# Kernel tuning notes

Measured on AMD Instinct MI355X. Metric: run time of the kernel, lower is better.

The kernel has to match this reference:

```python
import math
import jax, jax.numpy as jnp
import numpy as np

N_TOKENS = 2048
HIDDEN = 2880
HEAD_DIM = 64
N_HEADS = 64
N_KV = 8
Q_MULT = N_HEADS // N_KV  # 8
SLIDING_WINDOW = 128      # layer_idx=0 -> even -> window active
RMS_EPS = 1e-5
SM_SCALE = 1.0 / math.sqrt(HEAD_DIM)
ROPE_THETA = 150000.0
INIT_CTX = 4096
SCALING_FACTOR = 32.0
NTK_ALPHA = 1.0
NTK_BETA = 32.0
QKV_DIM = HEAD_DIM * (N_HEADS + 2 * N_KV)  # 5120


def _rope_cos_sin(n_tokens):
    # YaRN/NTK-scaled inverse frequencies (scaling_factor > 1 branch)
    freq = ROPE_THETA ** (jnp.arange(0, HEAD_DIM, 2, dtype=jnp.float32) / HEAD_DIM)
    concentration = 0.1 * math.log(SCALING_FACTOR) + 1.0
    d_half = HEAD_DIM / 2
    low = d_half * math.log(INIT_CTX / (NTK_BETA * 2 * math.pi)) / math.log(ROPE_THETA)
    high = d_half * math.log(INIT_CTX / (NTK_ALPHA * 2 * math.pi)) / math.log(ROPE_THETA)
    interpolation = 1.0 / (SCALING_FACTOR * freq)
    extrapolation = 1.0 / freq
    ramp = (jnp.arange(d_half, dtype=jnp.float32) - low) / (high - low)
    mask = 1.0 - jnp.clip(ramp, 0.0, 1.0)
    inv_freq = interpolation * (1.0 - mask) + extrapolation * mask
    pos = jnp.arange(n_tokens, dtype=jnp.float32)
    freqs = pos[:, None] * inv_freq[None, :]        # [n, d/2]
    return jnp.cos(freqs) * concentration, jnp.sin(freqs) * concentration


def _apply_rotary(x, cos, sin):
    # x: [n, h, d]; cos/sin: [n, d/2]
    c = cos[:, None, :]
    s = sin[:, None, :]
    x1, x2 = jnp.split(x, 2, axis=-1)
    return jnp.concatenate([x1 * c - x2 * s, x2 * c + x1 * s], axis=-1)


def setup_inputs() -> dict:
    key = jax.random.key(0)
    ks = jax.random.split(key, 4)
    x = jax.random.normal(ks[0], (N_TOKENS, HIDDEN), dtype=jnp.float32)
    norm_scale = jnp.ones((HIDDEN,), dtype=jnp.float32)
    sinks = jax.random.normal(ks[1], (N_HEADS,), dtype=jnp.float32)
    w_qkv = jax.random.normal(ks[2], (QKV_DIM, HIDDEN), dtype=jnp.float32) * 0.02
    b_qkv = jnp.zeros((QKV_DIM,), dtype=jnp.float32)
    w_out = jax.random.normal(ks[3], (HIDDEN, N_HEADS * HEAD_DIM), dtype=jnp.float32) * 0.02
    b_out = jnp.zeros((HIDDEN,), dtype=jnp.float32)
    return {"x": x, "norm_scale": norm_scale, "sinks": sinks,
            "w_qkv": w_qkv, "b_qkv": b_qkv, "w_out": w_out, "b_out": b_out}


def reference(x, norm_scale, sinks, w_qkv, b_qkv, w_out, b_out):
    n = x.shape[0]
    # RMSNorm (fp32 math as in original)
    t = x.astype(jnp.float32)
    t = t * jax.lax.rsqrt(jnp.mean(t * t, axis=-1, keepdims=True) + RMS_EPS)
    t = (t * norm_scale).astype(x.dtype)
    # QKV projection (torch Linear: y = x @ W^T + b)
    qkv = t @ w_qkv.T + b_qkv
    q = qkv[:, : N_HEADS * HEAD_DIM].reshape(n, N_KV, Q_MULT, HEAD_DIM)
    k = qkv[:, N_HEADS * HEAD_DIM:(N_HEADS + N_KV) * HEAD_DIM].reshape(n, N_KV, HEAD_DIM)
    v = qkv[:, (N_HEADS + N_KV) * HEAD_DIM:].reshape(n, N_KV, HEAD_DIM)
    # RoPE
    cos, sin = _rope_cos_sin(n)
    q = _apply_rotary(q.reshape(n, N_HEADS, HEAD_DIM), cos, sin).reshape(n, N_KV, Q_MULT, HEAD_DIM)
    k = _apply_rotary(k, cos, sin)
    # GQA attention scores: [kv_heads, q_mult, q, k]
    qk = jnp.einsum('qhmd,khd->hmqk', q, k) * SM_SCALE
    # causal + sliding-window mask: allow j <= i and j > i - SLIDING_WINDOW
    i = jnp.arange(n)[:, None]
    j = jnp.arange(n)[None, :]
    allowed = (j <= i) & (j > i - SLIDING_WINDOW)
    neg_inf = jnp.asarray(-jnp.inf, dtype=qk.dtype)
    qk = jnp.where(allowed[None, None, :, :], qk, neg_inf)
    # append learned sink logit per head, softmax, then drop sink column
    sink_logits = jnp.broadcast_to(
        sinks.reshape(N_KV, Q_MULT, 1, 1), (N_KV, Q_MULT, n, 1)).astype(qk.dtype)
    logits = jnp.concatenate([qk, sink_logits], axis=-1)
    weights = jax.nn.softmax(logits, axis=-1)[..., :-1]
    attn = jnp.einsum('hmqk,khd->qhmd', weights, v).reshape(n, N_HEADS * HEAD_DIM)
    return x + attn @ w_out.T + b_out
```

## Files before the change

### kernel.cpp

```cpp
#include <hip/hip_runtime.h>
#include <hip/hip_bf16.h>
#include <math.h>

typedef __attribute__((ext_vector_type(8))) short short8;
typedef __attribute__((ext_vector_type(4))) float f32x4;

#define NTOK 2048
#define HID  2880
#define QKVD 5120
#define KOFF 4096
#define VOFF 4608
#define ATTD 4096

__device__ __forceinline__ unsigned short f2bf(float f) {
  union { float f; unsigned int u; } v; v.f = f;
  unsigned int u = v.u;
  unsigned int r = (u + 0x7FFFu + ((u >> 16) & 1u)) >> 16;
  return (unsigned short)r;
}
__device__ __forceinline__ float bf2f(unsigned short h) {
  union { unsigned int u; float f; } v; v.u = ((unsigned int)h) << 16; return v.f;
}
__device__ __forceinline__ void gload_lds16(const unsigned short* g, unsigned short* l) {
  __builtin_amdgcn_global_load_lds(
      (const __attribute__((address_space(1))) unsigned int*)g,
      (__attribute__((address_space(3))) unsigned int*)l, 16, 0, 0);
}
#define MFMA16(a, b, c) __builtin_amdgcn_mfma_f32_16x16x32_bf16((a), (b), (c), 0, 0, 0)

__global__ __launch_bounds__(256) void prep_kernel(
    const float* __restrict__ x, const float* __restrict__ scale,
    unsigned short* __restrict__ t,
    const float* __restrict__ w1, unsigned short* __restrict__ w1bf,
    float* __restrict__ ctab, float* __restrict__ stab) {
  __shared__ float red[4];
  const int bid = blockIdx.x;
  const int tid = threadIdx.x;
  if (bid < 2048) {
    const float4* xr = (const float4*)(x + (size_t)bid * HID);
    const float4* sc = (const float4*)scale;
    float ss = 0.f;
    for (int c = tid; c < HID / 4; c += 256) {
      float4 v = xr[c];
      ss += v.x * v.x + v.y * v.y + v.z * v.z + v.w * v.w;
    }
    #pragma unroll
    for (int m = 1; m < 64; m <<= 1) ss += __shfl_xor(ss, m);
    if ((tid & 63) == 0) red[tid >> 6] = ss;
    __syncthreads();
    float tot = red[0] + red[1] + red[2] + red[3];
    float rs = rsqrtf(tot / (float)HID + 1e-5f);
    for (int c = tid; c < HID / 4; c += 256) {
      float4 v = xr[c];
      float4 s4 = sc[c];
      ushort4 o;
      o.x = f2bf(v.x * rs * s4.x); o.y = f2bf(v.y * rs * s4.y);
      o.z = f2bf(v.z * rs * s4.z); o.w = f2bf(v.w * rs * s4.w);
      *(ushort4*)&t[(size_t)bid * HID + c * 4] = o;
    }
  } else if (bid < 5648) {
    long base0 = (long)(bid - 2048) * 1024;
    #pragma unroll
    for (int k2 = 0; k2 < 4; ++k2) {
      long base = (base0 + k2 * 256 + tid) * 4;
      float4 v = *(const float4*)&w1[base];
      ushort4 o;
      o.x = f2bf(v.x); o.y = f2bf(v.y); o.z = f2bf(v.z); o.w = f2bf(v.w);
      *(ushort4*)&w1bf[base] = o;
    }
  } else {
    int idx = (bid - 5648) * 256 + tid;
    int pos = idx >> 5, i = idx & 31;
    const double theta = 150000.0;
    const double two_pi = 6.283185307179586476925286766559;
    double freq = pow(theta, (double)i / 32.0);
    double interp = 1.0 / (32.0 * freq);
    double extrap = 1.0 / freq;
    double low  = 32.0 * log(4096.0 / (32.0 * two_pi)) / log(theta);
    double high = 32.0 * log(4096.0 / (1.0  * two_pi)) / log(theta);
    double ramp = ((double)i - low) / (high - low);
    ramp = ramp < 0.0 ? 0.0 : (ramp > 1.0 ? 1.0 : ramp);
    double maskv = 1.0 - ramp;
    double inv = interp * (1.0 - maskv) + extrap * maskv;
    double ang = (double)pos * inv;
    double conc = 0.1 * log(32.0) + 1.0;
    ctab[idx] = (float)(cos(ang) * conc);
    stab[idx] = (float)(sin(ang) * conc);
  }
}

template<int BN, bool RESID>
__global__ __launch_bounds__(256, 2) void gemm_kernel(
    const unsigned short* __restrict__ A, const unsigned short* __restrict__ B,
    const float* __restrict__ bias, const float* __restrict__ resid,
    void* __restrict__ Cout, int K, int NC,
    const float* __restrict__ cvt_src, unsigned short* __restrict__ cvt_dst,
    int ngemm) {
  constexpr int NF = BN / 32;
  __shared__ unsigned short sA[2][8192];
  __shared__ unsigned short sB[2][BN * 64];

  const int tid = threadIdx.x;
  if ((int)blockIdx.x >= ngemm) {
    long base0 = (long)((int)blockIdx.x - ngemm) * 1024;
    #pragma unroll
    for (int k2 = 0; k2 < 4; ++k2) {
      long base = (base0 + k2 * 256 + tid) * 4;
      float4 v = *(const float4*)&cvt_src[base];
      ushort4 o;
      o.x = f2bf(v.x); o.y = f2bf(v.y); o.z = f2bf(v.z); o.w = f2bf(v.w);
      *(ushort4*)&cvt_dst[base] = o;
    }
    return;
  }
  const int q8 = ngemm >> 3;
  const int sw = ((int)blockIdx.x & 7) * q8 + ((int)blockIdx.x >> 3);
  const int m0 = (sw & 15) * 128;
  const int n0 = (sw >> 4) * BN;

  const int lane = tid & 63, wid = tid >> 6;
  const int fr = lane & 15, fq = lane >> 4;
  const int wr = wid >> 1, wc = wid & 1;
  const int swz = (fr & 7) << 4;
  const int r_st = tid >> 3;
  const int c8_st = ((tid & 7) ^ ((tid >> 3) & 7)) * 8;
  const int wlds = wid << 9;

  const unsigned short* Ag = A + (size_t)(m0 + r_st) * K + c8_st;
  const unsigned short* Bg = B + (size_t)(n0 + r_st) * K + c8_st;

  f32x4 acc[4][NF] = {};
  const int NT = K >> 6;

  auto LDA_ = [&](int bs, int mf, int ks) -> short8 {
    int row = wr * 64 + mf * 16 + fr;
    int cb = (ks * 64 + fq * 16) ^ swz;
    return *(const short8*)((const char*)&sA[bs][0] + row * 128 + cb);
  };
  auto LDB_ = [&](int bs, int nf, int ks) -> short8 {
    int row = wc * (NF * 16) + nf * 16 + fr;
    int cb = (ks * 64 + fq * 16) ^ swz;
    return *(const short8*)((const char*)&sB[bs][0] + row * 128 + cb);
  };
  auto issue_tile = [&](int tt, int b) {
    const unsigned short* Agt = Ag + (size_t)tt * 64;
    const unsigned short* Bgt = Bg + (size_t)tt * 64;
    #pragma unroll
    for (int s = 0; s < 4; ++s)
      gload_lds16(Agt + (size_t)(s * 32) * K, &sA[b][s * 2048 + wlds]);
    #pragma unroll
    for (int s = 0; s < NF; ++s)
      gload_lds16(Bgt + (size_t)(s * 32) * K, &sB[b][s * 2048 + wlds]);
  };

  issue_tile(0, 0);

  for (int t = 0; t < NT; ++t) {
    const int cu = t & 1;
    asm volatile("s_waitcnt vmcnt(0)" ::: "memory");
    __builtin_amdgcn_s_barrier();
    __builtin_amdgcn_sched_barrier(0);
    if (t + 1 < NT) issue_tile(t + 1, cu ^ 1);
    short8 afr0[4], bfr0[NF], afr1[4], bfr1[NF];
    #pragma unroll
    for (int mf = 0; mf < 4; ++mf) afr0[mf] = LDA_(cu, mf, 0);
    #pragma unroll
    for (int nf = 0; nf < NF; ++nf) bfr0[nf] = LDB_(cu, nf, 0);
    #pragma unroll
    for (int mf = 0; mf < 4; ++mf) afr1[mf] = LDA_(cu, mf, 1);
    #pragma unroll
    for (int nf = 0; nf < NF; ++nf) bfr1[nf] = LDB_(cu, nf, 1);
    __builtin_amdgcn_s_setprio(1);
    #pragma unroll
    for (int mf = 0; mf < 4; ++mf)
      #pragma unroll
      for (int nf = 0; nf < NF; ++nf)
        acc[mf][nf] = MFMA16(afr0[mf], bfr0[nf], acc[mf][nf]);
    #pragma unroll
    for (int mf = 0; mf < 4; ++mf)
      #pragma unroll
      for (int nf = 0; nf < NF; ++nf)
        acc[mf][nf] = MFMA16(afr1[mf], bfr1[nf], acc[mf][nf]);
    __builtin_amdgcn_s_setprio(0);
  }

  if (!RESID) {
    unsigned short* C = (unsigned short*)Cout;
    #pragma unroll
    for (int mf = 0; mf < 4; ++mf)
      #pragma unroll
      for (int nf = 0; nf < NF; ++nf)
        #pragma unroll
        for (int r = 0; r < 4; ++r) {
          int row = m0 + wr * 64 + mf * 16 + fq * 4 + r;
          int col = n0 + wc * (NF * 16) + nf * 16 + fr;
          C[(size_t)row * NC + col] = f2bf(acc[mf][nf][r] + bias[col]);
        }
  } else {
    float* C = (float*)Cout;
    #pragma unroll
    for (int mf = 0; mf < 4; ++mf)
      #pragma unroll
      for (int nf = 0; nf < NF; ++nf)
        #pragma unroll
        for (int r = 0; r < 4; ++r) {
          int row = m0 + wr * 64 + mf * 16 + fq * 4 + r;
          int col = n0 + wc * (NF * 16) + nf * 16 + fr;
          C[(size_t)row * NC + col] = acc[mf][nf][r] + bias[col] + resid[(size_t)row * NC + col];
        }
  }
}

__global__ __launch_bounds__(256) void attn_kernel(
    const unsigned short* __restrict__ qkv, const float* __restrict__ sinks,
    const float* __restrict__ ctab, const float* __restrict__ stab,
    unsigned short* __restrict__ attn) {
  const int tile = blockIdx.x;
  const int gh = blockIdx.y;
  const int h = gh >> 3;
  const int q0 = tile * 64;
  const int kbase = q0 - 127;

  __shared__ unsigned short Qsh[64][72];
  __shared__ unsigned short Ksh[192][72];
  __shared__ unsigned short Vt[64][200];
  __shared__ float rowpart[4][64];
  __shared__ float invsum[64];
  unsigned short (*Wsh)[200] = (unsigned short (*)[200])Ksh;

  const int tid = threadIdx.x;

  {
    int r = tid >> 2, cp = tid & 3;
    int i = q0 + r;
    const unsigned short* qp = &qkv[(size_t)i * QKVD + gh * 64 + cp * 8];
    short8 xa = *(const short8*)qp;
    short8 xb = *(const short8*)(qp + 32);
    short8 oa, ob;
    #pragma unroll
    for (int e = 0; e < 8; ++e) {
      float c = ctab[i * 32 + cp * 8 + e], s = stab[i * 32 + cp * 8 + e];
      float x1 = bf2f((unsigned short)xa[e]), x2 = bf2f((unsigned short)xb[e]);
      oa[e] = (short)f2bf(x1 * c - x2 * s);
      ob[e] = (short)f2bf(x2 * c + x1 * s);
    }
    *(short8*)&Qsh[r][cp * 8] = oa;
    *(short8*)&Qsh[r][cp * 8 + 32] = ob;
  }
  #pragma unroll
  for (int it = 0; it < 3; ++it) {
    int lin = tid + it * 256;
    int r = lin >> 2, cp = lin & 3;
    int j = kbase + r;
    short8 oa = {}, ob = {};
    if (j >= 0 && j < NTOK) {
      const unsigned short* kp = &qkv[(size_t)j * QKVD + KOFF + h * 64 + cp * 8];
      short8 xa = *(const short8*)kp;
      short8 xb = *(const short8*)(kp + 32);
      #pragma unroll
      for (int e = 0; e < 8; ++e) {
        float c = ctab[j * 32 + cp * 8 + e], s = stab[j * 32 + cp * 8 + e];
        float x1 = bf2f((unsigned short)xa[e]), x2 = bf2f((unsigned short)xb[e]);
        oa[e] = (short)f2bf(x1 * c - x2 * s);
        ob[e] = (short)f2bf(x2 * c + x1 * s);
      }
    }
    *(short8*)&Ksh[r][cp * 8] = oa;
    *(short8*)&Ksh[r][cp * 8 + 32] = ob;
  }
  #pragma unroll
  for (int c = 0; c < 6; ++c) {
    int lin = tid + c * 256;
    int r = lin >> 3, ch = (lin & 7) * 8;
    int j = kbase + r;
    uint4 v = make_uint4(0u, 0u, 0u, 0u);
    if (j >= 0 && j < NTOK) v = *(const uint4*)&qkv[(size_t)j * QKVD + VOFF + h * 64 + ch];
    const unsigned short* vs = (const unsigned short*)&v;
    #pragma unroll
    for (int i2 = 0; i2 < 8; ++i2) Vt[ch + i2][r] = vs[i2];
  }
  __syncthreads();

  const int lane = tid & 63;
  const int wid = tid >> 6;
  const int fr = lane & 15;
  const int fq = lane >> 4;
  const int fc = fq * 8;
  const int wk0 = wid * 48;

  f32x4 sc[4][3] = {};
  #pragma unroll
  for (int k0 = 0; k0 < 64; k0 += 32) {
    short8 qa[4], kb[3];
    #pragma unroll
    for (int mi = 0; mi < 4; ++mi) qa[mi] = *(const short8*)&Qsh[mi * 16 + fr][k0 + fc];
    #pragma unroll
    for (int ni = 0; ni < 3; ++ni) kb[ni] = *(const short8*)&Ksh[wk0 + ni * 16 + fr][k0 + fc];
    #pragma unroll
    for (int mi = 0; mi < 4; ++mi)
      #pragma unroll
      for (int ni = 0; ni < 3; ++ni)
        sc[mi][ni] = MFMA16(qa[mi], kb[ni], sc[mi][ni]);
  }

  float rsum[4][4];
  #pragma unroll
  for (int mi = 0; mi < 4; ++mi)
    #pragma unroll
    for (int r = 0; r < 4; ++r) {
      int i = q0 + mi * 16 + fq * 4 + r;
      float rs = 0.f;
      #pragma unroll
      for (int ni = 0; ni < 3; ++ni) {
        int kk = wk0 + ni * 16 + fr;
        int j = kbase + kk;
        bool valid = (j >= 0) && (j <= i) && (j > i - 128);
        float pw = valid ? __expf(sc[mi][ni][r] * 0.125f) : 0.f;
        sc[mi][ni][r] = pw;
        rs += pw;
      }
      rs += __shfl_xor(rs, 1);
      rs += __shfl_xor(rs, 2);
      rs += __shfl_xor(rs, 4);
      rs += __shfl_xor(rs, 8);
      rsum[mi][r] = rs;
    }

  __syncthreads();

  #pragma unroll
  for (int mi = 0; mi < 4; ++mi)
    #pragma unroll
    for (int r = 0; r < 4; ++r) {
      int row = mi * 16 + fq * 4 + r;
      #pragma unroll
      for (int ni = 0; ni < 3; ++ni)
        Wsh[row][wk0 + ni * 16 + fr] = f2bf(sc[mi][ni][r]);
      if (fr == 0) rowpart[wid][row] = rsum[mi][r];
    }
  __syncthreads();

  if (tid < 64) {
    float tot = rowpart[0][tid] + rowpart[1][tid] + rowpart[2][tid] + rowpart[3][tid];
    invsum[tid] = 1.f / (tot + __expf(sinks[gh]));
  }

  f32x4 pv[4] = {};
  #pragma unroll
  for (int k0 = 0; k0 < 192; k0 += 32) {
    short8 pa[4];
    #pragma unroll
    for (int mi = 0; mi < 4; ++mi) pa[mi] = *(const short8*)&Wsh[mi * 16 + fr][k0 + fc];
    short8 vb = *(const short8*)&Vt[wid * 16 + fr][k0 + fc];
    #pragma unroll
    for (int mi = 0; mi < 4; ++mi)
      pv[mi] = MFMA16(pa[mi], vb, pv[mi]);
  }
  __syncthreads();

  #pragma unroll
  for (int mi = 0; mi < 4; ++mi)
    #pragma unroll
    for (int r = 0; r < 4; ++r) {
      int row = mi * 16 + fq * 4 + r;
      float inv = invsum[row];
      int col = wid * 16 + fr;
      attn[(size_t)(q0 + row) * ATTD + gh * 64 + col] = f2bf(pv[mi][r] * inv);
    }
}

extern "C" void kernel_launch(void* const* d_in, const int* in_sizes, int n_in,
                              void* d_out, int out_size, void* d_ws, size_t ws_size,
                              hipStream_t stream) {
  const float* x          = (const float*)d_in[0];
  const float* norm_scale = (const float*)d_in[1];
  const float* sinks      = (const float*)d_in[2];
  const float* w_qkv      = (const float*)d_in[3];
  const float* b_qkv      = (const float*)d_in[4];
  const float* w_out      = (const float*)d_in[5];
  const float* b_out      = (const float*)d_in[6];
  float* out = (float*)d_out;

  char* ws = (char*)d_ws;
  unsigned short* qkv_bf = (unsigned short*)(ws);
  unsigned short* t_bf   = (unsigned short*)(ws + 20971520);
  unsigned short* attn_b = (unsigned short*)(ws + 20971520);
  unsigned short* w1bf   = (unsigned short*)(ws + 20971520 + 16777216);
  unsigned short* w2bf   = (unsigned short*)(ws + 20971520 + 16777216 + 29491200);
  float* ctab = (float*)(ws + 20971520 + 16777216 + 29491200 + 23592960);
  float* stab = ctab + NTOK * 32;

  prep_kernel<<<dim3(5904), dim3(256), 0, stream>>>(
      x, norm_scale, t_bf, w_qkv, w1bf, ctab, stab);
  gemm_kernel<160, false><<<dim3(3392), dim3(256), 0, stream>>>(
      t_bf, w1bf, b_qkv, nullptr, (void*)qkv_bf, HID, QKVD,
      w_out, w2bf, 512);
  attn_kernel<<<dim3(32, 64), dim3(256), 0, stream>>>(qkv_bf, sinks, ctab, stab, attn_b);
  gemm_kernel<96, true><<<dim3(480), dim3(256), 0, stream>>>(
      attn_b, w2bf, b_out, x, (void*)out, ATTD, HID,
      nullptr, nullptr, 480);
}
```

Measured before the change: 197.1 us.

## Interleave w_out bf16 conversion into QKV GEMM main loop

Measured after the change: 200.0 us. No clear change (+1.5%).

```diff
diff --git a/kernel.cpp b/kernel.cpp
--- a/kernel.cpp
+++ b/kernel.cpp
@@ -89,31 +89,19 @@
   }
 }
 
-template<int BN, bool RESID>
+template<int BN, bool RESID, bool CVT>
 __global__ __launch_bounds__(256, 2) void gemm_kernel(
     const unsigned short* __restrict__ A, const unsigned short* __restrict__ B,
     const float* __restrict__ bias, const float* __restrict__ resid,
     void* __restrict__ Cout, int K, int NC,
     const float* __restrict__ cvt_src, unsigned short* __restrict__ cvt_dst,
-    int ngemm) {
+    long cvt_nchunk) {
   constexpr int NF = BN / 32;
   __shared__ unsigned short sA[2][8192];
   __shared__ unsigned short sB[2][BN * 64];
 
   const int tid = threadIdx.x;
-  if ((int)blockIdx.x >= ngemm) {
-    long base0 = (long)((int)blockIdx.x - ngemm) * 1024;
-    #pragma unroll
-    for (int k2 = 0; k2 < 4; ++k2) {
-      long base = (base0 + k2 * 256 + tid) * 4;
-      float4 v = *(const float4*)&cvt_src[base];
-      ushort4 o;
-      o.x = f2bf(v.x); o.y = f2bf(v.y); o.z = f2bf(v.z); o.w = f2bf(v.w);
-      *(ushort4*)&cvt_dst[base] = o;
-    }
-    return;
-  }
-  const int q8 = ngemm >> 3;
+  const int q8 = gridDim.x >> 3;
   const int sw = ((int)blockIdx.x & 7) * q8 + ((int)blockIdx.x >> 3);
   const int m0 = (sw & 15) * 128;
   const int n0 = (sw >> 4) * BN;
@@ -152,8 +140,18 @@
     for (int s = 0; s < NF; ++s)
       gload_lds16(Bgt + (size_t)(s * 32) * K, &sB[b][s * 2048 + wlds]);
   };
+  float4 cv;
+  long cvbase = -1;
+  auto cvt_load = [&](int t) {
+    long chunk = (long)t * gridDim.x + (int)blockIdx.x;
+    if (chunk < cvt_nchunk) {
+      cvbase = chunk * 1024 + tid * 4;
+      cv = *(const float4*)&cvt_src[cvbase];
+    } else cvbase = -1;
+  };
 
   issue_tile(0, 0);
+  if (CVT) cvt_load(0);
 
   for (int t = 0; t < NT; ++t) {
     const int cu = t & 1;
@@ -161,6 +159,14 @@
     __builtin_amdgcn_s_barrier();
     __builtin_amdgcn_sched_barrier(0);
     if (t + 1 < NT) issue_tile(t + 1, cu ^ 1);
+    if (CVT) {
+      if (cvbase >= 0) {
+        ushort4 o;
+        o.x = f2bf(cv.x); o.y = f2bf(cv.y); o.z = f2bf(cv.z); o.w = f2bf(cv.w);
+        *(ushort4*)&cvt_dst[cvbase] = o;
+      }
+      if (t + 1 < NT) cvt_load(t + 1);
+    }
     short8 afr0[4], bfr0[NF], afr1[4], bfr1[NF];
     #pragma unroll
     for (int mf = 0; mf < 4; ++mf) afr0[mf] = LDA_(cu, mf, 0);
@@ -392,11 +398,11 @@
 
   prep_kernel<<<dim3(5904), dim3(256), 0, stream>>>(
       x, norm_scale, t_bf, w_qkv, w1bf, ctab, stab);
-  gemm_kernel<160, false><<<dim3(3392), dim3(256), 0, stream>>>(
+  gemm_kernel<160, false, true><<<dim3(512), dim3(256), 0, stream>>>(
       t_bf, w1bf, b_qkv, nullptr, (void*)qkv_bf, HID, QKVD,
-      w_out, w2bf, 512);
+      w_out, w2bf, 11520L);
   attn_kernel<<<dim3(32, 64), dim3(256), 0, stream>>>(qkv_bf, sinks, ctab, stab, attn_b);
-  gemm_kernel<96, true><<<dim3(480), dim3(256), 0, stream>>>(
+  gemm_kernel<96, true, false><<<dim3(480), dim3(256), 0, stream>>>(
       attn_b, w2bf, b_out, x, (void*)out, ATTD, HID,
-      nullptr, nullptr, 480);
-}
+      nullptr, nullptr, 0L);
+}
```
